# Kernel optimization log

Hardware: AMD Instinct MI355X
Metric: run time of the kernel (lower is better)

The kernel has to match this reference:

```python
import jax, jax.numpy as jnp
import numpy as np
import math

D_MODEL = 1024
N_HEADS = 16
D_K = D_MODEL // N_HEADS


def setup_inputs() -> dict:
    key = jax.random.key(0)
    ks = jax.random.split(key, 9)
    B, N = 2, 8192
    s = 1.0 / math.sqrt(D_MODEL)
    x = jax.random.normal(ks[0], (B, N, D_MODEL), dtype=jnp.float32)
    Wq = jax.random.normal(ks[1], (D_MODEL, D_MODEL), dtype=jnp.float32) * s
    bq = jnp.zeros((D_MODEL,), dtype=jnp.float32)
    Wk = jax.random.normal(ks[2], (D_MODEL, D_MODEL), dtype=jnp.float32) * s
    bk = jnp.zeros((D_MODEL,), dtype=jnp.float32)
    Wv = jax.random.normal(ks[3], (D_MODEL, D_MODEL), dtype=jnp.float32) * s
    bv = jnp.zeros((D_MODEL,), dtype=jnp.float32)
    Wo = jax.random.normal(ks[4], (D_MODEL, D_MODEL), dtype=jnp.float32) * s
    bo = jnp.zeros((D_MODEL,), dtype=jnp.float32)
    return {"x": x, "Wq": Wq, "bq": bq, "Wk": Wk, "bk": bk,
            "Wv": Wv, "bv": bv, "Wo": Wo, "bo": bo}


def _fft_circulant_attention(Q, K, V):
    # Q,K,V: (B,H,N,d_k); FFT along the sequence axis (axis=2)
    B, H, N, d_k = Q.shape
    scale = 1.0 / math.sqrt(d_k)
    Q_fft = jnp.fft.rfft(Q, axis=2)
    K_fft = jnp.fft.rfft(K, axis=2)
    # circular cross-correlation summed over d_k -> (B,H,Nf)
    scores_fft = jnp.sum(Q_fft * jnp.conj(K_fft), axis=-1)
    scores = jnp.fft.irfft(scores_fft, n=N, axis=2) * scale  # (B,H,N)
    attn = jax.nn.softmax(scores, axis=-1)                    # (B,H,N)
    attn_fft = jnp.fft.rfft(attn, axis=2)                     # (B,H,Nf)
    V_fft = jnp.fft.rfft(V, axis=2)                           # (B,H,Nf,d_k)
    out_fft = attn_fft[..., None] * V_fft
    return jnp.fft.irfft(out_fft, n=N, axis=2)                # (B,H,N,d_k)


def reference(x, Wq, bq, Wk, bk, Wv, bv, Wo, bo):
    B, N, _ = x.shape
    # torch Linear: x @ W.T + b
    def proj(W, b):
        return (x @ W.T + b).reshape(B, N, N_HEADS, D_K).transpose(0, 2, 1, 3)
    Q = proj(Wq, bq)
    K = proj(Wk, bk)
    V = proj(Wv, bv)
    O = _fft_circulant_attention(Q, K, V)          # (B,H,N,d_k)
    O = O.transpose(0, 2, 1, 3).reshape(B, N, D_MODEL)
    return O @ Wo.T + bo
```

## Files before the change

kernel.cpp:

```cpp
#include <hip/hip_runtime.h>
#include <math.h>
#include <stdint.h>

#define NDIM 8192
#define DM 1024
#define NH 16
#define DKH 64
#define BATCH 2
#define NSPLIT 16
#define NTF 256
#define NPTF (NDIM / NTF)

typedef __attribute__((ext_vector_type(8))) short short8v;
typedef __attribute__((ext_vector_type(4))) float f32x4;

__device__ inline float bf2f(unsigned short u) {
  return __uint_as_float(((unsigned int)u) << 16);
}
__device__ inline unsigned short f2bf(float f) {
  unsigned int u = __float_as_uint(f);
  u += 0x7fffu + ((u >> 16) & 1u);
  return (unsigned short)(u >> 16);
}
__device__ inline float2 cmul(float2 a, float2 b) {
  return make_float2(a.x * b.x - a.y * b.y, a.x * b.y + a.y * b.x);
}
__device__ inline float2 cmulc(float2 a, float2 b) {
  return make_float2(a.x * b.x + a.y * b.y, a.y * b.x - a.x * b.y);
}

__device__ inline void gload_lds16(const void* g, void* l) {
  __builtin_amdgcn_global_load_lds(
      (const __attribute__((address_space(1))) unsigned int*)(uintptr_t)g,
      (__attribute__((address_space(3))) unsigned int*)(uintptr_t)l, 16, 0, 0);
}

__global__ void twiddle_init(float2* tw) {
  int k = blockIdx.x * blockDim.x + threadIdx.x;
  if (k < NDIM) {
    double a = -2.0 * 3.14159265358979323846 * (double)k / (double)NDIM;
    tw[k] = make_float2((float)cos(a), (float)sin(a));
  }
}

__global__ __launch_bounds__(256)
void split_x(const float* __restrict__ x, unsigned short* __restrict__ xhi,
             unsigned short* __restrict__ xlo) {
  size_t i = ((size_t)blockIdx.x * 256 + threadIdx.x) * 4;
  float4 v = *(const float4*)&x[i];
  ushort4 h, l;
  h.x = f2bf(v.x); l.x = f2bf(v.x - bf2f(h.x));
  h.y = f2bf(v.y); l.y = f2bf(v.y - bf2f(h.y));
  h.z = f2bf(v.z); l.z = f2bf(v.z - bf2f(h.z));
  h.w = f2bf(v.w); l.w = f2bf(v.w - bf2f(h.w));
  *(ushort4*)&xhi[i] = h;
  *(ushort4*)&xlo[i] = l;
}

__global__ __launch_bounds__(256)
void split_w(const float* __restrict__ Wq, const float* __restrict__ Wk,
             const float* __restrict__ Wv, const float* __restrict__ Wo,
             unsigned short* __restrict__ whi, unsigned short* __restrict__ wlo,
             unsigned short* __restrict__ wob) {
  int z = blockIdx.z;
  const float* W = (z == 0) ? Wq : ((z == 1) ? Wk : ((z == 2) ? Wv : Wo));
  size_t i = ((size_t)blockIdx.x * 256 + threadIdx.x) * 4;
  float4 v = *(const float4*)&W[i];
  ushort4 h, l;
  h.x = f2bf(v.x); l.x = f2bf(v.x - bf2f(h.x));
  h.y = f2bf(v.y); l.y = f2bf(v.y - bf2f(h.y));
  h.z = f2bf(v.z); l.z = f2bf(v.z - bf2f(h.z));
  h.w = f2bf(v.w); l.w = f2bf(v.w - bf2f(h.w));
  if (z < 3) {
    *(ushort4*)&whi[(size_t)z * DM * DM + i] = h;
    *(ushort4*)&wlo[(size_t)z * DM * DM + i] = l;
  } else {
    *(ushort4*)&wob[i] = h;
  }
}

__device__ inline void fft_fwd(float2* __restrict__ s, const float2* __restrict__ tw, int tid) {
  const float C = 0.70710678118654752f;
  for (int lm = 10; lm >= 1; lm -= 3) {
    int m = 1 << lm;
    int sh = 10 - lm;
    __syncthreads();
    for (int t = tid; t < NDIM / 8; t += NTF) {
      int p = t & (m - 1);
      int i0 = ((t >> lm) << (lm + 3)) + p;
      float2 x0 = s[i0],       x1 = s[i0 + m],     x2 = s[i0 + 2 * m], x3 = s[i0 + 3 * m];
      float2 x4 = s[i0 + 4 * m], x5 = s[i0 + 5 * m], x6 = s[i0 + 6 * m], x7 = s[i0 + 7 * m];
      float2 e0 = {x0.x + x4.x, x0.y + x4.y}, o0 = {x0.x - x4.x, x0.y - x4.y};
      float2 e1 = {x1.x + x5.x, x1.y + x5.y}, o1 = {x1.x - x5.x, x1.y - x5.y};
      float2 e2 = {x2.x + x6.x, x2.y + x6.y}, o2 = {x2.x - x6.x, x2.y - x6.y};
      float2 e3 = {x3.x + x7.x, x3.y + x7.y}, o3 = {x3.x - x7.x, x3.y - x7.y};
      float2 t1 = {C * (o1.x + o1.y), C * (o1.y - o1.x)};
      float2 t2 = {o2.y, -o2.x};
      float2 t3 = {C * (o3.y - o3.x), -C * (o3.x + o3.y)};
      float2 pe = {e0.x + e2.x, e0.y + e2.y}, qe = {e0.x - e2.x, e0.y - e2.y};
      float2 re = {e1.x + e3.x, e1.y + e3.y}, se = {e1.x - e3.x, e1.y - e3.y};
      float2 po = {o0.x + t2.x, o0.y + t2.y}, qo = {o0.x - t2.x, o0.y - t2.y};
      float2 ro = {t1.x + t3.x, t1.y + t3.y}, so = {t1.x - t3.x, t1.y - t3.y};
      float2 y0 = {pe.x + re.x, pe.y + re.y};
      float2 y4 = {pe.x - re.x, pe.y - re.y};
      float2 y2 = {qe.x + se.y, qe.y - se.x};
      float2 y6 = {qe.x - se.y, qe.y + se.x};
      float2 y1 = {po.x + ro.x, po.y + ro.y};
      float2 y5 = {po.x - ro.x, po.y - ro.y};
      float2 y3 = {qo.x + so.y, qo.y - so.x};
      float2 y7 = {qo.x - so.y, qo.y + so.x};
      int e = p << sh;
      s[i0]         = y0;
      s[i0 + m]     = cmul(y1, tw[e]);
      s[i0 + 2 * m] = cmul(y2, tw[2 * e]);
      s[i0 + 3 * m] = cmul(y3, tw[3 * e]);
      s[i0 + 4 * m] = cmul(y4, tw[4 * e]);
      s[i0 + 5 * m] = cmul(y5, tw[5 * e]);
      s[i0 + 6 * m] = cmul(y6, tw[6 * e]);
      s[i0 + 7 * m] = cmul(y7, tw[7 * e]);
    }
  }
  __syncthreads();
  for (int t = tid; t < NDIM / 2; t += NTF) {
    int i0 = t * 2;
    float2 u = s[i0], v = s[i0 + 1];
    s[i0]     = make_float2(u.x + v.x, u.y + v.y);
    s[i0 + 1] = make_float2(u.x - v.x, u.y - v.y);
  }
  __syncthreads();
}

__device__ inline void fft_inv(float2* __restrict__ s, const float2* __restrict__ tw, int tid) {
  const float C = 0.70710678118654752f;
  __syncthreads();
  for (int t = tid; t < NDIM / 2; t += NTF) {
    int i0 = t * 2;
    float2 u = s[i0], v = s[i0 + 1];
    s[i0]     = make_float2(u.x + v.x, u.y + v.y);
    s[i0 + 1] = make_float2(u.x - v.x, u.y - v.y);
  }
  for (int lm = 1; lm <= 10; lm += 3) {
    int m = 1 << lm;
    int sh = 10 - lm;
    __syncthreads();
    for (int t = tid; t < NDIM / 8; t += NTF) {
      int p = t & (m - 1);
      int i0 = ((t >> lm) << (lm + 3)) + p;
      int e = p << sh;
      float2 z0 = s[i0];
      float2 z1 = cmulc(s[i0 + m],     tw[e]);
      float2 z2 = cmulc(s[i0 + 2 * m], tw[2 * e]);
      float2 z3 = cmulc(s[i0 + 3 * m], tw[3 * e]);
      float2 z4 = cmulc(s[i0 + 4 * m], tw[4 * e]);
      float2 z5 = cmulc(s[i0 + 5 * m], tw[5 * e]);
      float2 z6 = cmulc(s[i0 + 6 * m], tw[6 * e]);
      float2 z7 = cmulc(s[i0 + 7 * m], tw[7 * e]);
      float2 E0 = {z0.x + z4.x, z0.y + z4.y}, O0 = {z0.x - z4.x, z0.y - z4.y};
      float2 E1 = {z1.x + z5.x, z1.y + z5.y}, O1 = {z1.x - z5.x, z1.y - z5.y};
      float2 E2 = {z2.x + z6.x, z2.y + z6.y}, O2 = {z2.x - z6.x, z2.y - z6.y};
      float2 E3 = {z3.x + z7.x, z3.y + z7.y}, O3 = {z3.x - z7.x, z3.y - z7.y};
      float2 T1 = {C * (O1.x - O1.y), C * (O1.x + O1.y)};
      float2 T2 = {-O2.y, O2.x};
      float2 T3 = {-C * (O3.x + O3.y), C * (O3.x - O3.y)};
      float2 PE = {E0.x + E2.x, E0.y + E2.y}, QE = {E0.x - E2.x, E0.y - E2.y};
      float2 RE = {E1.x + E3.x, E1.y + E3.y}, SE = {E1.x - E3.x, E1.y - E3.y};
      float2 PO = {O0.x + T2.x, O0.y + T2.y}, QO = {O0.x - T2.x, O0.y - T2.y};
      float2 RO = {T1.x + T3.x, T1.y + T3.y}, SO = {T1.x - T3.x, T1.y - T3.y};
      s[i0]         = make_float2(PE.x + RE.x, PE.y + RE.y);
      s[i0 + 4 * m] = make_float2(PE.x - RE.x, PE.y - RE.y);
      s[i0 + 2 * m] = make_float2(QE.x - SE.y, QE.y + SE.x);
      s[i0 + 6 * m] = make_float2(QE.x + SE.y, QE.y - SE.x);
      s[i0 + m]     = make_float2(PO.x + RO.x, PO.y + RO.y);
      s[i0 + 5 * m] = make_float2(PO.x - RO.x, PO.y - RO.y);
      s[i0 + 3 * m] = make_float2(QO.x - SO.y, QO.y + SO.x);
      s[i0 + 7 * m] = make_float2(QO.x + SO.y, QO.y - SO.x);
    }
  }
  __syncthreads();
}

__device__ inline float blk_max(float v, float* red, int tid) {
  #pragma unroll
  for (int o = 32; o > 0; o >>= 1) v = fmaxf(v, __shfl_down(v, o, 64));
  __syncthreads();
  if ((tid & 63) == 0) red[tid >> 6] = v;
  __syncthreads();
  float r = fmaxf(fmaxf(red[0], red[1]), fmaxf(red[2], red[3]));
  __syncthreads();
  return r;
}
__device__ inline float blk_sum(float v, float* red, int tid) {
  #pragma unroll
  for (int o = 32; o > 0; o >>= 1) v += __shfl_down(v, o, 64);
  __syncthreads();
  if ((tid & 63) == 0) red[tid >> 6] = v;
  __syncthreads();
  float r = (red[0] + red[1]) + (red[2] + red[3]);
  __syncthreads();
  return r;
}

__global__ __launch_bounds__(512, 2)
void proj_gemm_mfma(const unsigned short* __restrict__ xhi, const unsigned short* __restrict__ xlo,
                    const unsigned short* __restrict__ whi, const unsigned short* __restrict__ wlo,
                    const float* __restrict__ bq, const float* __restrict__ bk,
                    const float* __restrict__ bv,
                    float* __restrict__ Qt, float* __restrict__ Kt, unsigned short* __restrict__ Vt) {
  extern __shared__ unsigned short smem[];
  int z = blockIdx.z;
  int b = z / 3, wsel = z % 3;
  bool full = (wsel < 2);
  const unsigned short* Wh = whi + (size_t)wsel * DM * DM;
  const unsigned short* Wl = wlo + (size_t)wsel * DM * DM;
  const float* bias = (wsel == 0) ? bq : ((wsel == 1) ? bk : bv);
  int cb = blockIdx.y * 128;
  int nb = blockIdx.x * 128;
  int tid = threadIdx.x;
  int lane = tid & 63, wid = tid >> 6;
  int wr = wid >> 2, wc = wid & 3;
  int srow = tid >> 3, sg = tid & 7;
  const unsigned short* gAh = Wh + (size_t)cb * DM;
  const unsigned short* gAl = Wl + (size_t)cb * DM;
  const unsigned short* gBh = xhi + ((size_t)b * NDIM + nb) * DM;
  const unsigned short* gBl = xlo + ((size_t)b * NDIM + nb) * DM;

  f32x4 acc[4][2];
  #pragma unroll
  for (int i = 0; i < 4; ++i)
    #pragma unroll
    for (int j = 0; j < 2; ++j) acc[i][j] = (f32x4){0.f, 0.f, 0.f, 0.f};

  int col = lane & 15, kg = lane >> 4;

  auto stage = [&](int buf, int k0) {
    unsigned short* base = smem + buf * 32768;
    #pragma unroll
    for (int i = 0; i < 2; ++i) {
      int r = i * 64 + srow;
      int gc = (sg ^ (r & 7)) * 8;
      size_t go = (size_t)r * DM + k0 + gc;
      int lo_ = r * 64 + sg * 8;
      gload_lds16(gAh + go, base + lo_);
      gload_lds16(gBh + go, base + 8192 + lo_);
      if (full) {
        gload_lds16(gAl + go, base + 16384 + lo_);
        gload_lds16(gBl + go, base + 24576 + lo_);
      }
    }
  };

  stage(0, 0);
  __syncthreads();
  int cur = 0;
  for (int t = 0; t < 16; ++t) {
    if (t < 15) stage(cur ^ 1, (t + 1) * 64);
    const unsigned short* pAh = smem + cur * 32768;
    const unsigned short* pBh = pAh + 8192;
    const unsigned short* pAl = pAh + 16384;
    const unsigned short* pBl = pAh + 24576;
    #pragma unroll
    for (int kk = 0; kk < 2; ++kk) {
      short8v ah[4], al[4], bh_[2], bl_[2];
      #pragma unroll
      for (int mi = 0; mi < 4; ++mi) {
        int r = wr * 64 + mi * 16 + col;
        int s = r * 64 + (((kk * 4 + kg) ^ (r & 7)) * 8);
        ah[mi] = *(const short8v*)&pAh[s];
        if (full) al[mi] = *(const short8v*)&pAl[s];
      }
      #pragma unroll
      for (int ni = 0; ni < 2; ++ni) {
        int r = wc * 32 + ni * 16 + col;
        int s = r * 64 + (((kk * 4 + kg) ^ (r & 7)) * 8);
        bh_[ni] = *(const short8v*)&pBh[s];
        if (full) bl_[ni] = *(const short8v*)&pBl[s];
      }
      #pragma unroll
      for (int mi = 0; mi < 4; ++mi)
        #pragma unroll
        for (int ni = 0; ni < 2; ++ni) {
          acc[mi][ni] = __builtin_amdgcn_mfma_f32_16x16x32_bf16(ah[mi], bh_[ni], acc[mi][ni], 0, 0, 0);
          if (full) {
            acc[mi][ni] = __builtin_amdgcn_mfma_f32_16x16x32_bf16(ah[mi], bl_[ni], acc[mi][ni], 0, 0, 0);
            acc[mi][ni] = __builtin_amdgcn_mfma_f32_16x16x32_bf16(al[mi], bh_[ni], acc[mi][ni], 0, 0, 0);
          }
        }
    }
    __syncthreads();
    cur ^= 1;
  }
  size_t obase = (size_t)b * DM * NDIM;
  #pragma unroll
  for (int mi = 0; mi < 4; ++mi) {
    #pragma unroll
    for (int reg = 0; reg < 4; ++reg) {
      int c = cb + wr * 64 + mi * 16 + kg * 4 + reg;
      float bsv = bias[c];
      #pragma unroll
      for (int ni = 0; ni < 2; ++ni) {
        int n = nb + wc * 32 + ni * 16 + col;
        float v = acc[mi][ni][reg] + bsv;
        if (wsel < 2) {
          float* out = ((wsel == 0) ? Qt : Kt) + obase;
          out[(size_t)c * NDIM + n] = v;
        } else {
          Vt[obase + (size_t)c * NDIM + n] = f2bf(v);
        }
      }
    }
  }
}

__global__ __launch_bounds__(256)
void score_fft_kernel(const float* __restrict__ Qt, const float* __restrict__ Kt,
                      const float2* __restrict__ tw, float2* __restrict__ part) {
  extern __shared__ float2 buf[];
  int bh = blockIdx.x / NSPLIT;
  int split = blockIdx.x % NSPLIT;
  int b = bh / NH, h = bh % NH;
  int tid = threadIdx.x;
  float qfx[NPTF], qfy[NPTF], accx[NPTF], accy[NPTF];
  #pragma unroll
  for (int i = 0; i < NPTF; ++i) { accx[i] = 0.f; accy[i] = 0.f; }

  for (int dp = 0; dp < 2; ++dp) {
    int c0 = h * DKH + (split * 2 + dp) * 2;
    const float* q0 = Qt + ((size_t)b * DM + c0) * NDIM;
    const float* q1 = q0 + NDIM;
    const float* k0c = Kt + ((size_t)b * DM + c0) * NDIM;
    const float* k1c = k0c + NDIM;
    #pragma unroll
    for (int i = 0; i < NPTF; ++i) {
      int ii = i * NTF + tid;
      buf[ii] = make_float2(q0[ii], q1[ii]);
    }
    fft_fwd(buf, tw, tid);
    #pragma unroll
    for (int i = 0; i < NPTF; ++i) { float2 v = buf[i * NTF + tid]; qfx[i] = v.x; qfy[i] = v.y; }
    #pragma unroll
    for (int i = 0; i < NPTF; ++i) {
      int ii = i * NTF + tid;
      buf[ii] = make_float2(k0c[ii], k1c[ii]);
    }
    fft_fwd(buf, tw, tid);
    #pragma unroll
    for (int i = 0; i < NPTF; ++i) {
      float2 kf = buf[i * NTF + tid];
      accx[i] += qfx[i] * kf.x + qfy[i] * kf.y;
      accy[i] += qfy[i] * kf.x - qfx[i] * kf.y;
    }
  }
  float2* dst = part + ((size_t)bh * NSPLIT + split) * NDIM;
  #pragma unroll
  for (int i = 0; i < NPTF; ++i) dst[i * NTF + tid] = make_float2(accx[i], accy[i]);
}

__global__ __launch_bounds__(256)
void reduce_part(const float2* __restrict__ part, float2* __restrict__ sred) {
  #pragma unroll
  for (int rep = 0; rep < 2; ++rep) {
    size_t g = (size_t)blockIdx.x * 512 + rep * 256 + threadIdx.x;
    int bh = (int)(g >> 13);
    int i  = (int)(g & (NDIM - 1));
    float sx = 0.f, sy = 0.f;
    #pragma unroll
    for (int s = 0; s < NSPLIT; ++s) {
      float2 v = part[((size_t)bh * NSPLIT + s) * NDIM + i];
      sx += v.x; sy += v.y;
    }
    sred[g] = make_float2(sx, sy);
  }
}

__global__ __launch_bounds__(256)
void softmax_attn_kernel(const float2* __restrict__ sred, const float2* __restrict__ tw,
                         float2* __restrict__ attnf) {
  extern __shared__ float2 buf[];
  int bh = blockIdx.x;
  int tid = threadIdx.x;
  for (int i = tid; i < NDIM; i += NTF) buf[i] = sred[(size_t)bh * NDIM + i];
  fft_inv(buf, tw, tid);
  const float scale = 0.125f / (float)NDIM;
  float vals[NPTF];
  float lmax = -3.0e38f;
  #pragma unroll
  for (int i = 0; i < NPTF; ++i) {
    float v = buf[i * NTF + tid].x * scale;
    vals[i] = v;
    lmax = fmaxf(lmax, v);
  }
  float* red = (float*)buf;
  float gmax = blk_max(lmax, red, tid);
  float lsum = 0.f;
  #pragma unroll
  for (int i = 0; i < NPTF; ++i) { float e = expf(vals[i] - gmax); vals[i] = e; lsum += e; }
  float gsum = blk_sum(lsum, red, tid);
  float inv = 1.0f / gsum;
  #pragma unroll
  for (int i = 0; i < NPTF; ++i) buf[i * NTF + tid] = make_float2(vals[i] * inv, 0.f);
  fft_fwd(buf, tw, tid);
  for (int i = tid; i < NDIM; i += NTF) attnf[(size_t)bh * NDIM + i] = buf[i];
}

__global__ __launch_bounds__(256)
void out_fft_kernel(const unsigned short* __restrict__ Vt, const float2* __restrict__ attnf,
                    const float2* __restrict__ tw, unsigned short* __restrict__ Ot) {
  extern __shared__ float2 buf[];
  int idx = blockIdx.x;
  int b = idx / (DM / 2), cp = idx % (DM / 2);
  int c0 = cp * 2;
  int h = c0 >> 6;
  int bh = b * NH + h;
  int tid = threadIdx.x;
  const unsigned short* v0 = Vt + ((size_t)b * DM + c0) * NDIM;
  const unsigned short* v1 = v0 + NDIM;
  for (int i = tid; i < NDIM; i += NTF) buf[i] = make_float2(bf2f(v0[i]), bf2f(v1[i]));
  fft_fwd(buf, tw, tid);
  for (int i = tid; i < NDIM; i += NTF) {
    float2 vf = buf[i];
    float2 af = attnf[(size_t)bh * NDIM + i];
    buf[i] = cmul(vf, af);
  }
  fft_inv(buf, tw, tid);
  const float invn = 1.0f / (float)NDIM;
  unsigned short* o0 = Ot + ((size_t)b * DM + c0) * NDIM;
  unsigned short* o1 = o0 + NDIM;
  for (int i = tid; i < NDIM; i += NTF) {
    float2 v = buf[i];
    o0[i] = f2bf(v.x * invn);
    o1[i] = f2bf(v.y * invn);
  }
}

__global__ __launch_bounds__(256)
void transpose_ot(const unsigned short* __restrict__ Ot, unsigned short* __restrict__ Ont) {
  int b = blockIdx.z;
  int cb = blockIdx.y * 64, n0 = blockIdx.x * 64;
  __shared__ unsigned short t[64][68];
  int tid = threadIdx.x;
  int r = tid >> 4, c4 = (tid & 15) * 4;
  const unsigned short* src = Ot + (size_t)b * DM * NDIM;
  #pragma unroll
  for (int i = 0; i < 4; ++i) {
    ushort4 v = *(const ushort4*)&src[(size_t)(cb + i * 16 + r) * NDIM + n0 + c4];
    *(ushort4*)&t[i * 16 + r][c4] = v;
  }
  __syncthreads();
  unsigned short* dst = Ont + (size_t)b * NDIM * DM;
  #pragma unroll
  for (int i = 0; i < 4; ++i) {
    int n = i * 16 + r;
    ushort4 v;
    v.x = t[c4 + 0][n]; v.y = t[c4 + 1][n]; v.z = t[c4 + 2][n]; v.w = t[c4 + 3][n];
    *(ushort4*)&dst[(size_t)(n0 + n) * DM + cb + c4] = v;
  }
}

__global__ __launch_bounds__(512, 2)
void final_gemm_mfma(const unsigned short* __restrict__ Ont, const unsigned short* __restrict__ Wob,
                     const float* __restrict__ bo, float* __restrict__ out) {
  extern __shared__ unsigned short smem[];
  int b = blockIdx.z;
  int nb = blockIdx.x * 128;
  int pb = blockIdx.y * 128;
  int tid = threadIdx.x;
  int lane = tid & 63, wid = tid >> 6;
  int wr = wid >> 2, wc = wid & 3;
  int srow = tid >> 3, sg = tid & 7;
  const unsigned short* gA = Ont + ((size_t)b * NDIM + nb) * DM;
  const unsigned short* gB = Wob + (size_t)pb * DM;

  f32x4 acc[4][2];
  #pragma unroll
  for (int i = 0; i < 4; ++i)
    #pragma unroll
    for (int j = 0; j < 2; ++j) acc[i][j] = (f32x4){0.f, 0.f, 0.f, 0.f};

  int col = lane & 15, kg = lane >> 4;

  auto stage = [&](int buf, int k0) {
    unsigned short* base = smem + buf * 16384;
    #pragma unroll
    for (int i = 0; i < 2; ++i) {
      int r = i * 64 + srow;
      int gc = (sg ^ (r & 7)) * 8;
      size_t go = (size_t)r * DM + k0 + gc;
      int lo_ = r * 64 + sg * 8;
      gload_lds16(gA + go, base + lo_);
      gload_lds16(gB + go, base + 8192 + lo_);
    }
  };

  stage(0, 0);
  __syncthreads();
  int cur = 0;
  for (int t = 0; t < 16; ++t) {
    if (t < 15) stage(cur ^ 1, (t + 1) * 64);
    const unsigned short* pA = smem + cur * 16384;
    const unsigned short* pB = pA + 8192;
    #pragma unroll
    for (int kk = 0; kk < 2; ++kk) {
      short8v af[4], bf[2];
      #pragma unroll
      for (int mi = 0; mi < 4; ++mi) {
        int r = wr * 64 + mi * 16 + col;
        af[mi] = *(const short8v*)&pA[r * 64 + (((kk * 4 + kg) ^ (r & 7)) * 8)];
      }
      #pragma unroll
      for (int ni = 0; ni < 2; ++ni) {
        int r = wc * 32 + ni * 16 + col;
        bf[ni] = *(const short8v*)&pB[r * 64 + (((kk * 4 + kg) ^ (r & 7)) * 8)];
      }
      #pragma unroll
      for (int mi = 0; mi < 4; ++mi)
        #pragma unroll
        for (int ni = 0; ni < 2; ++ni)
          acc[mi][ni] = __builtin_amdgcn_mfma_f32_16x16x32_bf16(af[mi], bf[ni], acc[mi][ni], 0, 0, 0);
    }
    __syncthreads();
    cur ^= 1;
  }
  #pragma unroll
  for (int mi = 0; mi < 4; ++mi) {
    #pragma unroll
    for (int reg = 0; reg < 4; ++reg) {
      int n = nb + wr * 64 + mi * 16 + kg * 4 + reg;
      size_t rowoff = ((size_t)b * NDIM + n) * DM;
      #pragma unroll
      for (int ni = 0; ni < 2; ++ni) {
        int cp = pb + wc * 32 + ni * 16 + col;
        out[rowoff + cp] = acc[mi][ni][reg] + bo[cp];
      }
    }
  }
}

extern "C" void kernel_launch(void* const* d_in, const int* in_sizes, int n_in,
                              void* d_out, int out_size, void* d_ws, size_t ws_size,
                              hipStream_t stream) {
  (void)in_sizes; (void)n_in; (void)out_size;
  const float* x  = (const float*)d_in[0];
  const float* Wq = (const float*)d_in[1]; const float* bq = (const float*)d_in[2];
  const float* Wk = (const float*)d_in[3]; const float* bk = (const float*)d_in[4];
  const float* Wv = (const float*)d_in[5]; const float* bv = (const float*)d_in[6];
  const float* Wo = (const float*)d_in[7]; const float* bo = (const float*)d_in[8];

  char* ws = (char*)d_ws;
  size_t off = 0;
  float2* tw = (float2*)(ws + off); off += (size_t)NDIM * sizeof(float2);
  float*  Qt = (float*)(ws + off);  off += (size_t)BATCH * DM * NDIM * 4;
  float*  Kt = (float*)(ws + off);  off += (size_t)BATCH * DM * NDIM * 4;
  unsigned short* Vt  = (unsigned short*)(ws + off); off += (size_t)BATCH * DM * NDIM * 2;
  size_t xhi_off = off;
  unsigned short* Xhi = (unsigned short*)(ws + off); off += (size_t)BATCH * NDIM * DM * 2;
  size_t xlo_off = off;
  unsigned short* Xlo = (unsigned short*)(ws + off); off += (size_t)BATCH * NDIM * DM * 2;
  unsigned short* Whi = (unsigned short*)(ws + off); off += (size_t)3 * DM * DM * 2;
  unsigned short* Wlo = (unsigned short*)(ws + off); off += (size_t)3 * DM * DM * 2;
  unsigned short* Wob = (unsigned short*)(ws + off); off += (size_t)DM * DM * 2;
  float2* part  = (float2*)(ws + xhi_off);
  float2* attnf = (float2*)(ws + xlo_off);
  float2* sred  = (float2*)(ws + xlo_off + 4194304);
  unsigned short* Ot  = (unsigned short*)Qt;
  unsigned short* Ont = (unsigned short*)Kt;

  if (ws_size < off) return;

  twiddle_init<<<32, 256, 0, stream>>>(tw);
  split_x<<<(BATCH * NDIM * DM) / (256 * 4), 256, 0, stream>>>(x, Xhi, Xlo);
  split_w<<<dim3((DM * DM) / (256 * 4), 1, 4), 256, 0, stream>>>(Wq, Wk, Wv, Wo, Whi, Wlo, Wob);

  dim3 pg(NDIM / 128, DM / 128, 3 * BATCH);
  proj_gemm_mfma<<<pg, 512, 131072, stream>>>(Xhi, Xlo, Whi, Wlo, bq, bk, bv, Qt, Kt, Vt);

  score_fft_kernel<<<BATCH * NH * NSPLIT, NTF, NDIM * sizeof(float2), stream>>>(Qt, Kt, tw, part);
  reduce_part<<<(BATCH * NH * NDIM) / 512, 256, 0, stream>>>(part, sred);
  softmax_attn_kernel<<<BATCH * NH, NTF, NDIM * sizeof(float2), stream>>>(sred, tw, attnf);
  out_fft_kernel<<<BATCH * DM / 2, NTF, NDIM * sizeof(float2), stream>>>(Vt, attnf, tw, Ot);

  transpose_ot<<<dim3(NDIM / 64, DM / 64, BATCH), 256, 0, stream>>>(Ot, Ont);
  final_gemm_mfma<<<dim3(NDIM / 128, DM / 128, BATCH), 512, 65536, stream>>>(Ont, Wob, bo, (float*)d_out);
}
```

Measured before the change: 543.3 us.

## Drop double buffering in projection and output GEMMs for higher occupancy and block swizzle

Both MFMA GEMMs change from a double-buffered dynamic-LDS pipeline to a single-buffered static-LDS loop that waits on vmcnt(0) and a barrier each k-step. This halves shared memory per block, and launch bounds rise to 4 blocks per CU so other resident blocks can hide load latency instead of in-block prefetch. The grids become 1D with an XCD-style swizzle that groups neighbouring tiles on the same chiplet to improve L2 reuse. The risk is exposed global-load latency per iteration and register pressure from the tighter launch bound.

```diff
diff --git a/kernel.cpp b/kernel.cpp
--- a/kernel.cpp
+++ b/kernel.cpp
@@ -200,21 +200,24 @@
   return r;
 }
 
-__global__ __launch_bounds__(512, 2)
+__global__ __launch_bounds__(512, 4)
 void proj_gemm_mfma(const unsigned short* __restrict__ xhi, const unsigned short* __restrict__ xlo,
                     const unsigned short* __restrict__ whi, const unsigned short* __restrict__ wlo,
                     const float* __restrict__ bq, const float* __restrict__ bk,
                     const float* __restrict__ bv,
                     float* __restrict__ Qt, float* __restrict__ Kt, unsigned short* __restrict__ Vt) {
-  extern __shared__ unsigned short smem[];
-  int z = blockIdx.z;
+  int raw = blockIdx.x;
+  int swz = (raw & 7) * 384 + (raw >> 3);
+  int nb = (swz & 63) * 128;
+  int cb = ((swz >> 6) & 7) * 128;
+  int z  = swz >> 9;
   int b = z / 3, wsel = z % 3;
   bool full = (wsel < 2);
   const unsigned short* Wh = whi + (size_t)wsel * DM * DM;
   const unsigned short* Wl = wlo + (size_t)wsel * DM * DM;
   const float* bias = (wsel == 0) ? bq : ((wsel == 1) ? bk : bv);
-  int cb = blockIdx.y * 128;
-  int nb = blockIdx.x * 128;
+  __shared__ unsigned short lAh[128 * 64], lAl[128 * 64];
+  __shared__ unsigned short lBh[128 * 64], lBl[128 * 64];
   int tid = threadIdx.x;
   int lane = tid & 63, wid = tid >> 6;
   int wr = wid >> 2, wc = wid & 3;
@@ -231,33 +234,22 @@
     for (int j = 0; j < 2; ++j) acc[i][j] = (f32x4){0.f, 0.f, 0.f, 0.f};
 
   int col = lane & 15, kg = lane >> 4;
-
-  auto stage = [&](int buf, int k0) {
-    unsigned short* base = smem + buf * 32768;
+  for (int k0 = 0; k0 < DM; k0 += 64) {
     #pragma unroll
     for (int i = 0; i < 2; ++i) {
       int r = i * 64 + srow;
       int gc = (sg ^ (r & 7)) * 8;
       size_t go = (size_t)r * DM + k0 + gc;
       int lo_ = r * 64 + sg * 8;
-      gload_lds16(gAh + go, base + lo_);
-      gload_lds16(gBh + go, base + 8192 + lo_);
+      gload_lds16(gAh + go, &lAh[lo_]);
+      gload_lds16(gBh + go, &lBh[lo_]);
       if (full) {
-        gload_lds16(gAl + go, base + 16384 + lo_);
-        gload_lds16(gBl + go, base + 24576 + lo_);
-      }
-    }
-  };
-
-  stage(0, 0);
-  __syncthreads();
-  int cur = 0;
-  for (int t = 0; t < 16; ++t) {
-    if (t < 15) stage(cur ^ 1, (t + 1) * 64);
-    const unsigned short* pAh = smem + cur * 32768;
-    const unsigned short* pBh = pAh + 8192;
-    const unsigned short* pAl = pAh + 16384;
-    const unsigned short* pBl = pAh + 24576;
+        gload_lds16(gAl + go, &lAl[lo_]);
+        gload_lds16(gBl + go, &lBl[lo_]);
+      }
+    }
+    asm volatile("s_waitcnt vmcnt(0)");
+    __syncthreads();
     #pragma unroll
     for (int kk = 0; kk < 2; ++kk) {
       short8v ah[4], al[4], bh_[2], bl_[2];
@@ -265,15 +257,15 @@
       for (int mi = 0; mi < 4; ++mi) {
         int r = wr * 64 + mi * 16 + col;
         int s = r * 64 + (((kk * 4 + kg) ^ (r & 7)) * 8);
-        ah[mi] = *(const short8v*)&pAh[s];
-        if (full) al[mi] = *(const short8v*)&pAl[s];
+        ah[mi] = *(const short8v*)&lAh[s];
+        if (full) al[mi] = *(const short8v*)&lAl[s];
       }
       #pragma unroll
       for (int ni = 0; ni < 2; ++ni) {
         int r = wc * 32 + ni * 16 + col;
         int s = r * 64 + (((kk * 4 + kg) ^ (r & 7)) * 8);
-        bh_[ni] = *(const short8v*)&pBh[s];
-        if (full) bl_[ni] = *(const short8v*)&pBl[s];
+        bh_[ni] = *(const short8v*)&lBh[s];
+        if (full) bl_[ni] = *(const short8v*)&lBl[s];
       }
       #pragma unroll
       for (int mi = 0; mi < 4; ++mi)
@@ -287,7 +279,6 @@
         }
     }
     __syncthreads();
-    cur ^= 1;
   }
   size_t obase = (size_t)b * DM * NDIM;
   #pragma unroll
@@ -456,13 +447,15 @@
   }
 }
 
-__global__ __launch_bounds__(512, 2)
+__global__ __launch_bounds__(512, 4)
 void final_gemm_mfma(const unsigned short* __restrict__ Ont, const unsigned short* __restrict__ Wob,
                      const float* __restrict__ bo, float* __restrict__ out) {
-  extern __shared__ unsigned short smem[];
-  int b = blockIdx.z;
-  int nb = blockIdx.x * 128;
-  int pb = blockIdx.y * 128;
+  int raw = blockIdx.x;
+  int swz = (raw & 7) * 128 + (raw >> 3);
+  int nb = (swz & 63) * 128;
+  int pb = ((swz >> 6) & 7) * 128;
+  int b  = swz >> 9;
+  __shared__ unsigned short lA[128 * 64], lB[128 * 64];
   int tid = threadIdx.x;
   int lane = tid & 63, wid = tid >> 6;
   int wr = wid >> 2, wc = wid & 3;
@@ -477,39 +470,30 @@
     for (int j = 0; j < 2; ++j) acc[i][j] = (f32x4){0.f, 0.f, 0.f, 0.f};
 
   int col = lane & 15, kg = lane >> 4;
-
-  auto stage = [&](int buf, int k0) {
-    unsigned short* base = smem + buf * 16384;
+  for (int k0 = 0; k0 < DM; k0 += 64) {
     #pragma unroll
     for (int i = 0; i < 2; ++i) {
       int r = i * 64 + srow;
       int gc = (sg ^ (r & 7)) * 8;
       size_t go = (size_t)r * DM + k0 + gc;
       int lo_ = r * 64 + sg * 8;
-      gload_lds16(gA + go, base + lo_);
-      gload_lds16(gB + go, base + 8192 + lo_);
-    }
-  };
-
-  stage(0, 0);
-  __syncthreads();
-  int cur = 0;
-  for (int t = 0; t < 16; ++t) {
-    if (t < 15) stage(cur ^ 1, (t + 1) * 64);
-    const unsigned short* pA = smem + cur * 16384;
-    const unsigned short* pB = pA + 8192;
+      gload_lds16(gA + go, &lA[lo_]);
+      gload_lds16(gB + go, &lB[lo_]);
+    }
+    asm volatile("s_waitcnt vmcnt(0)");
+    __syncthreads();
     #pragma unroll
     for (int kk = 0; kk < 2; ++kk) {
       short8v af[4], bf[2];
       #pragma unroll
       for (int mi = 0; mi < 4; ++mi) {
         int r = wr * 64 + mi * 16 + col;
-        af[mi] = *(const short8v*)&pA[r * 64 + (((kk * 4 + kg) ^ (r & 7)) * 8)];
+        af[mi] = *(const short8v*)&lA[r * 64 + (((kk * 4 + kg) ^ (r & 7)) * 8)];
       }
       #pragma unroll
       for (int ni = 0; ni < 2; ++ni) {
         int r = wc * 32 + ni * 16 + col;
-        bf[ni] = *(const short8v*)&pB[r * 64 + (((kk * 4 + kg) ^ (r & 7)) * 8)];
+        bf[ni] = *(const short8v*)&lB[r * 64 + (((kk * 4 + kg) ^ (r & 7)) * 8)];
       }
       #pragma unroll
       for (int mi = 0; mi < 4; ++mi)
@@ -518,7 +502,6 @@
           acc[mi][ni] = __builtin_amdgcn_mfma_f32_16x16x32_bf16(af[mi], bf[ni], acc[mi][ni], 0, 0, 0);
     }
     __syncthreads();
-    cur ^= 1;
   }
   #pragma unroll
   for (int mi = 0; mi < 4; ++mi) {
@@ -570,8 +553,7 @@
   split_x<<<(BATCH * NDIM * DM) / (256 * 4), 256, 0, stream>>>(x, Xhi, Xlo);
   split_w<<<dim3((DM * DM) / (256 * 4), 1, 4), 256, 0, stream>>>(Wq, Wk, Wv, Wo, Whi, Wlo, Wob);
 
-  dim3 pg(NDIM / 128, DM / 128, 3 * BATCH);
-  proj_gemm_mfma<<<pg, 512, 131072, stream>>>(Xhi, Xlo, Whi, Wlo, bq, bk, bv, Qt, Kt, Vt);
+  proj_gemm_mfma<<<3072, 512, 0, stream>>>(Xhi, Xlo, Whi, Wlo, bq, bk, bv, Qt, Kt, Vt);
 
   score_fft_kernel<<<BATCH * NH * NSPLIT, NTF, NDIM * sizeof(float2), stream>>>(Qt, Kt, tw, part);
   reduce_part<<<(BATCH * NH * NDIM) / 512, 256, 0, stream>>>(part, sred);
@@ -579,5 +561,5 @@
   out_fft_kernel<<<BATCH * DM / 2, NTF, NDIM * sizeof(float2), stream>>>(Vt, attnf, tw, Ot);
 
   transpose_ot<<<dim3(NDIM / 64, DM / 64, BATCH), 256, 0, stream>>>(Ot, Ont);
-  final_gemm_mfma<<<dim3(NDIM / 128, DM / 128, BATCH), 512, 65536, stream>>>(Ont, Wob, bo, (float*)d_out);
-}
+  final_gemm_mfma<<<1024, 512, 0, stream>>>(Ont, Wob, bo, (float*)d_out);
+}
```

New measurement: 571.3 us. +5.2%, slower.
